# Kernel tuning notes

Hardware: AMD Instinct MI355X
Metric: run time of the kernel (lower is better)

## Reference

```python
import jax, jax.numpy as jnp
import numpy as np

NB_HEAD = 8
SIZE_PER_HEAD = 64
MAX_LEN = 1024
D_IN = 512
BATCH = 8
NEG_BIG = 1e12  # matches the torch module's mask * 1000000000000.0


def setup_inputs() -> dict:
    key = jax.random.key(0)
    ks = jax.random.split(key, 6)
    return {
        "Q_seq": jax.random.normal(ks[0], (BATCH, MAX_LEN, D_IN), dtype=jnp.float32),
        "K_seq": jax.random.normal(ks[1], (BATCH, MAX_LEN, D_IN), dtype=jnp.float32),
        "V_seq": jax.random.normal(ks[2], (BATCH, MAX_LEN, D_IN), dtype=jnp.float32),
        "WQ": jax.random.normal(ks[3], (D_IN, NB_HEAD * SIZE_PER_HEAD), dtype=jnp.float32),
        "WK": jax.random.normal(ks[4], (D_IN, NB_HEAD * SIZE_PER_HEAD), dtype=jnp.float32),
        "WV": jax.random.normal(ks[5], (D_IN, NB_HEAD * SIZE_PER_HEAD), dtype=jnp.float32),
    }


def reference(Q_seq, K_seq, V_seq, WQ, WK, WV):
    B, L, _ = Q_seq.shape
    H, D = NB_HEAD, SIZE_PER_HEAD
    # QKV projections -> [B, H, L, D]
    q = (Q_seq @ WQ).reshape(B, L, H, D).transpose(0, 2, 1, 3)
    k = (K_seq @ WK).reshape(B, L, H, D).transpose(0, 2, 1, 3)
    v = (V_seq @ WV).reshape(B, L, H, D).transpose(0, 2, 1, 3)
    # scaled dot-product scores [B, H, Lq, Lk]
    scores = jnp.einsum("bhqd,bhkd->bhqk", q, k) / jnp.sqrt(jnp.float32(D))
    # causal mask: the torch Mask() subtracts 1e12 where key_idx > query_idx
    causal = jnp.triu(jnp.ones((L, L), dtype=scores.dtype), k=1)  # 1 where k > q
    scores = scores - causal[None, None, :, :] * NEG_BIG
    attn = jax.nn.softmax(scores, axis=-1)
    out = jnp.einsum("bhqk,bhkd->bhqd", attn, v)  # [B, H, L, D]
    return out.transpose(0, 2, 1, 3).reshape(B, L, H * D)
```

## Files before the change

### kernel.cpp

```cpp
#include <hip/hip_runtime.h>
#include <cstddef>

#define LEN    1024
#define DIN    512
#define NHEAD  8
#define HDIM   64
#define BATCH  8

typedef __attribute__((ext_vector_type(8))) short  short8;
typedef __attribute__((ext_vector_type(4))) float  f32x4;

#define MFMA16(a, b, c) __builtin_amdgcn_mfma_f32_16x16x32_bf16((a), (b), (c), 0, 0, 0)
#define PERM_HI 0x07060302u
#define PERM_LO 0x05040100u

__device__ __forceinline__ unsigned short bf_hi(float x) {
    unsigned u = __float_as_uint(x);
    return (unsigned short)((u + 0x7fffu + ((u >> 16) & 1u)) >> 16);
}
__device__ __forceinline__ void bf_split(float x, unsigned short& h, unsigned short& l) {
    unsigned u  = __float_as_uint(x);
    unsigned hu = (u + 0x7fffu + ((u >> 16) & 1u)) >> 16;
    h = (unsigned short)hu;
    l = bf_hi(x - __uint_as_float(hu << 16));
}
__device__ __forceinline__ void unpack4(uint4 u, ushort4& h, ushort4& l) {
    h = make_ushort4((unsigned short)(u.x >> 16), (unsigned short)(u.y >> 16),
                     (unsigned short)(u.z >> 16), (unsigned short)(u.w >> 16));
    l = make_ushort4((unsigned short)(u.x & 0xffff), (unsigned short)(u.y & 0xffff),
                     (unsigned short)(u.z & 0xffff), (unsigned short)(u.w & 0xffff));
}
__device__ __forceinline__ void unpack8(uint4 a, uint4 b, uint4& h, uint4& l) {
    h = make_uint4(__builtin_amdgcn_perm(a.y, a.x, PERM_HI),
                   __builtin_amdgcn_perm(a.w, a.z, PERM_HI),
                   __builtin_amdgcn_perm(b.y, b.x, PERM_HI),
                   __builtin_amdgcn_perm(b.w, b.z, PERM_HI));
    l = make_uint4(__builtin_amdgcn_perm(a.y, a.x, PERM_LO),
                   __builtin_amdgcn_perm(a.w, a.z, PERM_LO),
                   __builtin_amdgcn_perm(b.y, b.x, PERM_LO),
                   __builtin_amdgcn_perm(b.w, b.z, PERM_LO));
}

template<int CTRL>
__device__ __forceinline__ float dpp_mov(float x) {
    return __int_as_float(__builtin_amdgcn_update_dpp(
        0, __float_as_int(x), CTRL, 0xF, 0xF, true));
}
__device__ __forceinline__ float red16_max(float x) {
    x = fmaxf(x, dpp_mov<0xB1>(x));
    x = fmaxf(x, dpp_mov<0x4E>(x));
    x = fmaxf(x, dpp_mov<0x141>(x));
    x = fmaxf(x, dpp_mov<0x140>(x));
    return x;
}
__device__ __forceinline__ float red16_sum(float x) {
    x += dpp_mov<0xB1>(x);
    x += dpp_mov<0x4E>(x);
    x += dpp_mov<0x141>(x);
    x += dpp_mov<0x140>(x);
    return x;
}

__global__ __launch_bounds__(256)
void wprep(const float* __restrict__ WQ, const float* __restrict__ WK,
           const float* __restrict__ WV, unsigned short* __restrict__ wt)
{
    __shared__ float T[64][68];
    const int z = blockIdx.z;
    const float* W = (z == 0) ? WQ : (z == 1) ? WK : WV;
    unsigned short* Wth = wt + (size_t)z * 524288;
    unsigned short* Wtl = Wth + 262144;
    const int k0 = blockIdx.x * 64, n0 = blockIdx.y * 64;
    const int t = threadIdx.x;
    #pragma unroll
    for (int e = 0; e < 4; ++e) {
        int f = e * 256 + t, r = f >> 4, c4 = (f & 15) << 2;
        *(float4*)&T[r][c4] = *(const float4*)&W[(size_t)(k0 + r) * 512 + n0 + c4];
    }
    __syncthreads();
    #pragma unroll
    for (int e = 0; e < 4; ++e) {
        int f = e * 256 + t, nr = f >> 4, kc4 = (f & 15) << 2;
        ushort4 h, l;
        bf_split(T[kc4 + 0][nr], h.x, l.x);
        bf_split(T[kc4 + 1][nr], h.y, l.y);
        bf_split(T[kc4 + 2][nr], h.z, l.z);
        bf_split(T[kc4 + 3][nr], h.w, l.w);
        *(ushort4*)&Wth[(size_t)(n0 + nr) * 512 + k0 + kc4] = h;
        *(ushort4*)&Wtl[(size_t)(n0 + nr) * 512 + k0 + kc4] = l;
    }
}

#define PSTR 40

__global__ __launch_bounds__(256, 3)
void proj_mfma(const float* __restrict__ Qin, const float* __restrict__ Kin,
               const float* __restrict__ Vin, const unsigned short* __restrict__ wt,
               unsigned int* __restrict__ qhl, unsigned int* __restrict__ khl,
               unsigned short* __restrict__ vh)
{
    __shared__ unsigned short Ah[128 * PSTR], Al[128 * PSTR],
                              Bh[128 * PSTR], Bl[128 * PSTR];
    const int z = blockIdx.z;
    const bool full = (z < 2);
    const float* X = (z == 0) ? Qin : (z == 1) ? Kin : Vin;
    const unsigned short* Wth = wt + (size_t)z * 524288;
    const unsigned short* Wtl = Wth + 262144;

    const int t = threadIdx.x, lane = t & 63, w = t >> 6;
    const int wm = w & 1, wn = w >> 1;
    const int m0 = blockIdx.x * 128, n0 = blockIdx.y * 128;
    const int lm = lane & 15, lq = lane >> 4;
    const int ar = t >> 1, ak = (t & 1) * 16;

    const float* Xp = X + (size_t)(m0 + ar) * 512 + ak;
    const unsigned short* Bph = Wth + (size_t)(n0 + ar) * 512 + ak;
    const unsigned short* Bpl = Wtl + (size_t)(n0 + ar) * 512 + ak;

    f32x4 acc[4][4];
    #pragma unroll
    for (int i = 0; i < 4; ++i)
        #pragma unroll
        for (int j = 0; j < 4; ++j) acc[i][j] = 0.f;

    float4 av[4];
    uint4 bh0, bh1, bl0, bl1;
    #pragma unroll
    for (int e = 0; e < 4; ++e) av[e] = *(const float4*)(Xp + e * 4);
    bh0 = *(const uint4*)(Bph);
    bh1 = *(const uint4*)(Bph + 8);
    if (full) { bl0 = *(const uint4*)(Bpl); bl1 = *(const uint4*)(Bpl + 8); }

    for (int k0 = 0; k0 < 512; k0 += 32) {
        __syncthreads();
        {
            const float* ff = (const float*)&av[0];
            uint hw[16];
            #pragma unroll
            for (int i = 0; i < 16; ++i) hw[i] = __float_as_uint(ff[i]) & 0xffff0000u;
            uint4 ahv  = make_uint4(__builtin_amdgcn_perm(hw[1],  hw[0],  PERM_HI),
                                    __builtin_amdgcn_perm(hw[3],  hw[2],  PERM_HI),
                                    __builtin_amdgcn_perm(hw[5],  hw[4],  PERM_HI),
                                    __builtin_amdgcn_perm(hw[7],  hw[6],  PERM_HI));
            uint4 ahv2 = make_uint4(__builtin_amdgcn_perm(hw[9],  hw[8],  PERM_HI),
                                    __builtin_amdgcn_perm(hw[11], hw[10], PERM_HI),
                                    __builtin_amdgcn_perm(hw[13], hw[12], PERM_HI),
                                    __builtin_amdgcn_perm(hw[15], hw[14], PERM_HI));
            *(uint4*)&Ah[ar * PSTR + ak]     = ahv;
            *(uint4*)&Ah[ar * PSTR + ak + 8] = ahv2;
            if (full) {
                uint lo[8];
                #pragma unroll
                for (int i = 0; i < 8; ++i) {
                    float r0 = ff[2*i]   - __uint_as_float(hw[2*i]);
                    float r1 = ff[2*i+1] - __uint_as_float(hw[2*i+1]);
                    lo[i] = ((uint)bf_hi(r1) << 16) | bf_hi(r0);
                }
                *(uint4*)&Al[ar * PSTR + ak]     = make_uint4(lo[0], lo[1], lo[2], lo[3]);
                *(uint4*)&Al[ar * PSTR + ak + 8] = make_uint4(lo[4], lo[5], lo[6], lo[7]);
            }
        }
        *(uint4*)&Bh[ar * PSTR + ak]     = bh0;
        *(uint4*)&Bh[ar * PSTR + ak + 8] = bh1;
        if (full) {
            *(uint4*)&Bl[ar * PSTR + ak]     = bl0;
            *(uint4*)&Bl[ar * PSTR + ak + 8] = bl1;
        }
        __syncthreads();

        if (k0 + 32 < 512) {
            #pragma unroll
            for (int e = 0; e < 4; ++e) av[e] = *(const float4*)(Xp + k0 + 32 + e * 4);
            bh0 = *(const uint4*)(Bph + k0 + 32);
            bh1 = *(const uint4*)(Bph + k0 + 40);
            if (full) {
                bl0 = *(const uint4*)(Bpl + k0 + 32);
                bl1 = *(const uint4*)(Bpl + k0 + 40);
            }
        }

        short8 a_h[4], a_l[4];
        #pragma unroll
        for (int mi = 0; mi < 4; ++mi) {
            int off = (wm * 64 + mi * 16 + lm) * PSTR + lq * 8;
            a_h[mi] = *(const short8*)&Ah[off];
            if (full) a_l[mi] = *(const short8*)&Al[off];
        }
        #pragma unroll
        for (int ni = 0; ni < 4; ++ni) {
            int off = (wn * 64 + ni * 16 + lm) * PSTR + lq * 8;
            short8 b_h = *(const short8*)&Bh[off];
            if (full) {
                short8 b_l = *(const short8*)&Bl[off];
                #pragma unroll
                for (int mi = 0; mi < 4; ++mi) {
                    acc[mi][ni] = MFMA16(a_l[mi], b_h, acc[mi][ni]);
                    acc[mi][ni] = MFMA16(a_h[mi], b_l, acc[mi][ni]);
                    acc[mi][ni] = MFMA16(a_h[mi], b_h, acc[mi][ni]);
                }
            } else {
                #pragma unroll
                for (int mi = 0; mi < 4; ++mi)
                    acc[mi][ni] = MFMA16(a_h[mi], b_h, acc[mi][ni]);
            }
        }
    }

    if (z < 2) {
        unsigned int* o = (z == 0) ? qhl : khl;
        const float sc = (z == 0) ? 0.18033688011112042f : 1.0f;
        #pragma unroll
        for (int mi = 0; mi < 4; ++mi)
            #pragma unroll
            for (int ni = 0; ni < 4; ++ni) {
                int n_abs = n0 + wn * 64 + ni * 16 + lm;
                int hd = n_abs >> 6, d = n_abs & 63;
                #pragma unroll
                for (int r = 0; r < 4; ++r) {
                    int m_abs = m0 + wm * 64 + mi * 16 + lq * 4 + r;
                    int b = m_abs >> 10, li = m_abs & 1023;
                    unsigned short hv, lv;
                    bf_split(acc[mi][ni][r] * sc, hv, lv);
                    o[(((size_t)b * NHEAD + hd) * LEN + li) * HDIM + d] =
                        ((unsigned)hv << 16) | lv;
                }
            }
    } else {
        #pragma unroll
        for (int mi = 0; mi < 4; ++mi) {
            int m_base = m0 + wm * 64 + mi * 16 + lq * 4;
            int b = m_base >> 10, l0 = m_base & 1023;
            #pragma unroll
            for (int ni = 0; ni < 4; ++ni) {
                int n_abs = n0 + wn * 64 + ni * 16 + lm;
                int hd = n_abs >> 6, d = n_abs & 63;
                ushort4 hv = make_ushort4(bf_hi(acc[mi][ni][0]), bf_hi(acc[mi][ni][1]),
                                          bf_hi(acc[mi][ni][2]), bf_hi(acc[mi][ni][3]));
                *(ushort4*)&vh[(((size_t)b * NHEAD + hd) * HDIM + d) * LEN + l0] = hv;
            }
        }
    }
}

__global__ __launch_bounds__(256)
void attn_mfma(const unsigned int* __restrict__ qhl, const unsigned int* __restrict__ khl,
               const unsigned short* __restrict__ vth, float* __restrict__ out)
{
    __shared__ unsigned short sm[18432];
    unsigned short* Kh  = sm;
    unsigned short* Kl  = sm + 4608;
    unsigned short* Pb  = sm;
    unsigned short* Vt  = sm + 9216;
    unsigned short* Qsh = sm;
    unsigned short* Qsl = sm + 9216;

    const int t = threadIdx.x, lane = t & 63, w = t >> 6;
    const int lm = lane & 15, lq = lane >> 4;
    const int bx = blockIdx.x;
    const int idx = bx >> 1, par = bx & 1;
    const int bh = idx & 63;
    const int a  = idx >> 6;
    const int qt = par ? (7 - a) : a;
    const size_t base = (size_t)bh * LEN * HDIM;
    const unsigned int*   qb = qhl + base;
    const unsigned int*   kb = khl + base;
    const unsigned short* vb = vth + base;
    const int Q0  = qt * 128;
    const int Q0w = Q0 + w * 32;

    #pragma unroll
    for (int e = 0; e < 8; ++e) {
        int f = e * 256 + t, r = f >> 4, c4 = (f & 15) << 2;
        uint4 u = *(const uint4*)&qb[(size_t)(Q0 + r) * 64 + c4];
        ushort4 h, l;
        unpack4(u, h, l);
        *(ushort4*)&Qsh[r * 72 + c4] = h;
        *(ushort4*)&Qsl[r * 72 + c4] = l;
    }
    __syncthreads();
    short8 qfh[2][2], qfl[2][2];
    #pragma unroll
    for (int mi = 0; mi < 2; ++mi)
        #pragma unroll
        for (int ks = 0; ks < 2; ++ks) {
            int off = (w * 32 + mi * 16 + lm) * 72 + ks * 32 + lq * 8;
            qfh[mi][ks] = *(const short8*)&Qsh[off];
            qfl[mi][ks] = *(const short8*)&Qsl[off];
        }

    float m_i[2][4], l_i[2][4];
    f32x4 oacc[2][4];
    #pragma unroll
    for (int mi = 0; mi < 2; ++mi)
        #pragma unroll
        for (int r = 0; r < 4; ++r) { m_i[mi][r] = -1e30f; l_i[mi][r] = 0.f; }
    #pragma unroll
    for (int mi = 0; mi < 2; ++mi)
        #pragma unroll
        for (int nd = 0; nd < 4; ++nd) oacc[mi][nd] = 0.f;

    const int kr = t >> 2, kq = t & 3;
    const int vd_ = t >> 3, vs8 = (t & 7) << 3;

    uint4 kreg[4], vreg[2];
    #pragma unroll
    for (int e = 0; e < 4; ++e)
        kreg[e] = *(const uint4*)&kb[(size_t)kr * 64 + kq * 16 + e * 4];
    #pragma unroll
    for (int e = 0; e < 2; ++e)
        vreg[e] = *(const uint4*)&vb[(size_t)(e * 32 + vd_) * LEN + vs8];

    const int jend = 2 * qt + 1;
    for (int jb = 0; jb <= jend; ++jb) {
        __syncthreads();
        {
            uint4 h0, l0, h1, l1;
            unpack8(kreg[0], kreg[1], h0, l0);
            unpack8(kreg[2], kreg[3], h1, l1);
            int ko = kr * 72 + kq * 16;
            *(uint4*)&Kh[ko]     = h0;
            *(uint4*)&Kh[ko + 8] = h1;
            *(uint4*)&Kl[ko]     = l0;
            *(uint4*)&Kl[ko + 8] = l1;
            *(uint4*)&Vt[(vd_)      * 72 + vs8] = vreg[0];
            *(uint4*)&Vt[(vd_ + 32) * 72 + vs8] = vreg[1];
        }
        __syncthreads();

        if (jb < jend) {
            #pragma unroll
            for (int e = 0; e < 4; ++e)
                kreg[e] = *(const uint4*)&kb[(size_t)((jb + 1) * 64 + kr) * 64 + kq * 16 + e * 4];
            #pragma unroll
            for (int e = 0; e < 2; ++e)
                vreg[e] = *(const uint4*)&vb[(size_t)(e * 32 + vd_) * LEN + (jb + 1) * 64 + vs8];
        }

        const bool active = (jb * 64 <= Q0w + 31);
        f32x4 sf[2][4];
        if (active) {
            #pragma unroll
            for (int mi = 0; mi < 2; ++mi)
                #pragma unroll
                for (int ni = 0; ni < 4; ++ni) sf[mi][ni] = 0.f;
            #pragma unroll
            for (int ks = 0; ks < 2; ++ks)
                #pragma unroll
                for (int ni = 0; ni < 4; ++ni) {
                    int off = (ni * 16 + lm) * 72 + ks * 32 + lq * 8;
                    short8 b_h = *(const short8*)&Kh[off];
                    short8 b_l = *(const short8*)&Kl[off];
                    #pragma unroll
                    for (int mi = 0; mi < 2; ++mi) {
                        sf[mi][ni] = MFMA16(qfl[mi][ks], b_h, sf[mi][ni]);
                        sf[mi][ni] = MFMA16(qfh[mi][ks], b_l, sf[mi][ni]);
                        sf[mi][ni] = MFMA16(qfh[mi][ks], b_h, sf[mi][ni]);
                    }
                }
            if (jb * 64 + 63 > Q0w) {
                #pragma unroll
                for (int mi = 0; mi < 2; ++mi)
                    #pragma unroll
                    for (int ni = 0; ni < 4; ++ni) {
                        int key = jb * 64 + ni * 16 + lm;
                        #pragma unroll
                        for (int r = 0; r < 4; ++r) {
                            int qi = Q0w + mi * 16 + lq * 4 + r;
                            if (key > qi) sf[mi][ni][r] = -1e30f;
                        }
                    }
            }
        }
        __syncthreads();

        if (active) {
            #pragma unroll
            for (int mi = 0; mi < 2; ++mi)
                #pragma unroll
                for (int r = 0; r < 4; ++r) {
                    float mv = fmaxf(fmaxf(sf[mi][0][r], sf[mi][1][r]),
                                     fmaxf(sf[mi][2][r], sf[mi][3][r]));
                    mv = red16_max(mv);
                    float mo = m_i[mi][r];
                    float mn = fmaxf(mo, mv);
                    float al = __builtin_amdgcn_exp2f(mo - mn);
                    m_i[mi][r] = mn;
                    float rs = 0.f;
                    int prow = (w * 32 + mi * 16 + lq * 4 + r) * 72 + lm;
                    #pragma unroll
                    for (int ni = 0; ni < 4; ++ni) {
                        float p = __builtin_amdgcn_exp2f(sf[mi][ni][r] - mn);
                        rs += p;
                        Pb[prow + ni * 16] = bf_hi(p);
                    }
                    rs = red16_sum(rs);
                    l_i[mi][r] = l_i[mi][r] * al + rs;
                    #pragma unroll
                    for (int nd = 0; nd < 4; ++nd) oacc[mi][nd][r] *= al;
                }
            short8 pf[2][2];
            #pragma unroll
            for (int mi = 0; mi < 2; ++mi)
                #pragma unroll
                for (int ks = 0; ks < 2; ++ks)
                    pf[mi][ks] = *(const short8*)&Pb[(w * 32 + mi * 16 + lm) * 72 + ks * 32 + lq * 8];
            #pragma unroll
            for (int ks = 0; ks < 2; ++ks)
                #pragma unroll
                for (int nd = 0; nd < 4; ++nd) {
                    short8 vf = *(const short8*)&Vt[(nd * 16 + lm) * 72 + ks * 32 + lq * 8];
                    #pragma unroll
                    for (int mi = 0; mi < 2; ++mi)
                        oacc[mi][nd] = MFMA16(pf[mi][ks], vf, oacc[mi][nd]);
                }
        }
    }

    const int b = bh >> 3, hd = bh & 7;
    #pragma unroll
    for (int mi = 0; mi < 2; ++mi)
        #pragma unroll
        for (int r = 0; r < 4; ++r) {
            int qrow = Q0w + mi * 16 + lq * 4 + r;
            float inv = 1.0f / l_i[mi][r];
            #pragma unroll
            for (int nd = 0; nd < 4; ++nd) {
                int d = nd * 16 + lm;
                out[((size_t)b * LEN + qrow) * (NHEAD * HDIM) + hd * 64 + d] =
                    oacc[mi][nd][r] * inv;
            }
        }
}

extern "C" void kernel_launch(void* const* d_in, const int* in_sizes, int n_in,
                              void* d_out, int out_size, void* d_ws, size_t ws_size,
                              hipStream_t stream)
{
    const float* Qin = (const float*)d_in[0];
    const float* Kin = (const float*)d_in[1];
    const float* Vin = (const float*)d_in[2];
    const float* WQ  = (const float*)d_in[3];
    const float* WK  = (const float*)d_in[4];
    const float* WV  = (const float*)d_in[5];

    const size_t per = (size_t)BATCH * NHEAD * LEN * HDIM;
    unsigned int*   qhl = (unsigned int*)d_ws;
    unsigned int*   khl = qhl + per;
    unsigned short* vh  = (unsigned short*)(khl + per);
    unsigned short* wt  = vh + per;

    wprep    <<<dim3(8, 8, 3),  256, 0, stream>>>(WQ, WK, WV, wt);
    proj_mfma<<<dim3(64, 4, 3), 256, 0, stream>>>(Qin, Kin, Vin, wt, qhl, khl, vh);
    attn_mfma<<<dim3(512),      256, 0, stream>>>(qhl, khl, vh, (float*)d_out);
}
```

Before: 185.4 us.

## Pre-split activations into bf16 hi/lo in a separate pass before projection GEMM

Adds an xprep kernel that converts the Q/K/V fp32 activations once into bf16 high and low halves in workspace. The projection GEMM then loads ready-made bf16 tiles instead of reading fp32 and splitting them inside every tile. Previously each activation row was re-read and re-split by all four N-blocks, so this removes repeated conversion work and halves the bytes loaded per tile. In exchange it adds an extra launch plus a write and re-read of the split activations. LDS stride drops from 40 to 36 and occupancy hint rises from 3 to 4 blocks.

Result: slower. 288.8 us (+55.8%).

```diff
diff --git a/kernel.cpp b/kernel.cpp
--- a/kernel.cpp
+++ b/kernel.cpp
@@ -91,11 +91,41 @@
     }
 }
 
-#define PSTR 40
-
-__global__ __launch_bounds__(256, 3)
-void proj_mfma(const float* __restrict__ Qin, const float* __restrict__ Kin,
-               const float* __restrict__ Vin, const unsigned short* __restrict__ wt,
+__global__ __launch_bounds__(256)
+void xprep(const float* __restrict__ Qin, const float* __restrict__ Kin,
+           const float* __restrict__ Vin,
+           unsigned short* __restrict__ xh, unsigned short* __restrict__ xl)
+{
+    const int z = blockIdx.y;
+    const float* X = (z == 0) ? Qin : (z == 1) ? Kin : Vin;
+    unsigned short* H = xh + (size_t)z * (8192 * 512);
+    unsigned short* L = xl + (size_t)z * (8192 * 512);
+    const size_t i = ((size_t)blockIdx.x * 256 + threadIdx.x) * 8;
+    float4 a = *(const float4*)&X[i];
+    float4 b = *(const float4*)&X[i + 4];
+    ushort4 h0, l0, h1, l1;
+    bf_split(a.x, h0.x, l0.x);
+    bf_split(a.y, h0.y, l0.y);
+    bf_split(a.z, h0.z, l0.z);
+    bf_split(a.w, h0.w, l0.w);
+    bf_split(b.x, h1.x, l1.x);
+    bf_split(b.y, h1.y, l1.y);
+    bf_split(b.z, h1.z, l1.z);
+    bf_split(b.w, h1.w, l1.w);
+    *(ushort4*)&H[i]     = h0;
+    *(ushort4*)&H[i + 4] = h1;
+    if (z < 2) {
+        *(ushort4*)&L[i]     = l0;
+        *(ushort4*)&L[i + 4] = l1;
+    }
+}
+
+#define PSTR 36
+
+__global__ __launch_bounds__(256, 4)
+void proj_mfma(const unsigned short* __restrict__ xh,
+               const unsigned short* __restrict__ xl,
+               const unsigned short* __restrict__ wt,
                unsigned int* __restrict__ qhl, unsigned int* __restrict__ khl,
                unsigned short* __restrict__ vh)
 {
@@ -103,7 +133,8 @@
                               Bh[128 * PSTR], Bl[128 * PSTR];
     const int z = blockIdx.z;
     const bool full = (z < 2);
-    const float* X = (z == 0) ? Qin : (z == 1) ? Kin : Vin;
+    const unsigned short* Xh  = xh + (size_t)z * (8192 * 512);
+    const unsigned short* Xl  = xl + (size_t)z * (8192 * 512);
     const unsigned short* Wth = wt + (size_t)z * 524288;
     const unsigned short* Wtl = Wth + 262144;
 
@@ -113,7 +144,8 @@
     const int lm = lane & 15, lq = lane >> 4;
     const int ar = t >> 1, ak = (t & 1) * 16;
 
-    const float* Xp = X + (size_t)(m0 + ar) * 512 + ak;
+    const unsigned short* Aph = Xh  + (size_t)(m0 + ar) * 512 + ak;
+    const unsigned short* Apl = Xl  + (size_t)(m0 + ar) * 512 + ak;
     const unsigned short* Bph = Wth + (size_t)(n0 + ar) * 512 + ak;
     const unsigned short* Bpl = Wtl + (size_t)(n0 + ar) * 512 + ak;
 
@@ -123,59 +155,42 @@
         #pragma unroll
         for (int j = 0; j < 4; ++j) acc[i][j] = 0.f;
 
-    float4 av[4];
-    uint4 bh0, bh1, bl0, bl1;
-    #pragma unroll
-    for (int e = 0; e < 4; ++e) av[e] = *(const float4*)(Xp + e * 4);
-    bh0 = *(const uint4*)(Bph);
-    bh1 = *(const uint4*)(Bph + 8);
-    if (full) { bl0 = *(const uint4*)(Bpl); bl1 = *(const uint4*)(Bpl + 8); }
+    uint4 pah0, pah1, pbh0, pbh1, pal0, pal1, pbl0, pbl1;
+    pah0 = *(const uint4*)(Aph);
+    pah1 = *(const uint4*)(Aph + 8);
+    pbh0 = *(const uint4*)(Bph);
+    pbh1 = *(const uint4*)(Bph + 8);
+    if (full) {
+        pal0 = *(const uint4*)(Apl);
+        pal1 = *(const uint4*)(Apl + 8);
+        pbl0 = *(const uint4*)(Bpl);
+        pbl1 = *(const uint4*)(Bpl + 8);
+    }
 
     for (int k0 = 0; k0 < 512; k0 += 32) {
         __syncthreads();
-        {
-            const float* ff = (const float*)&av[0];
-            uint hw[16];
-            #pragma unroll
-            for (int i = 0; i < 16; ++i) hw[i] = __float_as_uint(ff[i]) & 0xffff0000u;
-            uint4 ahv  = make_uint4(__builtin_amdgcn_perm(hw[1],  hw[0],  PERM_HI),
-                                    __builtin_amdgcn_perm(hw[3],  hw[2],  PERM_HI),
-                                    __builtin_amdgcn_perm(hw[5],  hw[4],  PERM_HI),
-                                    __builtin_amdgcn_perm(hw[7],  hw[6],  PERM_HI));
-            uint4 ahv2 = make_uint4(__builtin_amdgcn_perm(hw[9],  hw[8],  PERM_HI),
-                                    __builtin_amdgcn_perm(hw[11], hw[10], PERM_HI),
-                                    __builtin_amdgcn_perm(hw[13], hw[12], PERM_HI),
-                                    __builtin_amdgcn_perm(hw[15], hw[14], PERM_HI));
-            *(uint4*)&Ah[ar * PSTR + ak]     = ahv;
-            *(uint4*)&Ah[ar * PSTR + ak + 8] = ahv2;
+        *(uint4*)&Ah[ar * PSTR + ak]     = pah0;
+        *(uint4*)&Ah[ar * PSTR + ak + 8] = pah1;
+        *(uint4*)&Bh[ar * PSTR + ak]     = pbh0;
+        *(uint4*)&Bh[ar * PSTR + ak + 8] = pbh1;
+        if (full) {
+            *(uint4*)&Al[ar * PSTR + ak]     = pal0;
+            *(uint4*)&Al[ar * PSTR + ak + 8] = pal1;
+            *(uint4*)&Bl[ar * PSTR + ak]     = pbl0;
+            *(uint4*)&Bl[ar * PSTR + ak + 8] = pbl1;
+        }
+        __syncthreads();
+
+        if (k0 + 32 < 512) {
+            pah0 = *(const uint4*)(Aph + k0 + 32);
+            pah1 = *(const uint4*)(Aph + k0 + 40);
+            pbh0 = *(const uint4*)(Bph + k0 + 32);
+            pbh1 = *(const uint4*)(Bph + k0 + 40);
             if (full) {
-                uint lo[8];
-                #pragma unroll
-                for (int i = 0; i < 8; ++i) {
-                    float r0 = ff[2*i]   - __uint_as_float(hw[2*i]);
-                    float r1 = ff[2*i+1] - __uint_as_float(hw[2*i+1]);
-                    lo[i] = ((uint)bf_hi(r1) << 16) | bf_hi(r0);
-                }
-                *(uint4*)&Al[ar * PSTR + ak]     = make_uint4(lo[0], lo[1], lo[2], lo[3]);
-                *(uint4*)&Al[ar * PSTR + ak + 8] = make_uint4(lo[4], lo[5], lo[6], lo[7]);
-            }
-        }
-        *(uint4*)&Bh[ar * PSTR + ak]     = bh0;
-        *(uint4*)&Bh[ar * PSTR + ak + 8] = bh1;
-        if (full) {
-            *(uint4*)&Bl[ar * PSTR + ak]     = bl0;
-            *(uint4*)&Bl[ar * PSTR + ak + 8] = bl1;
-        }
-        __syncthreads();
-
-        if (k0 + 32 < 512) {
-            #pragma unroll
-            for (int e = 0; e < 4; ++e) av[e] = *(const float4*)(Xp + k0 + 32 + e * 4);
-            bh0 = *(const uint4*)(Bph + k0 + 32);
-            bh1 = *(const uint4*)(Bph + k0 + 40);
-            if (full) {
-                bl0 = *(const uint4*)(Bpl + k0 + 32);
-                bl1 = *(const uint4*)(Bpl + k0 + 40);
+                pal0 = *(const uint4*)(Apl + k0 + 32);
+                pal1 = *(const uint4*)(Apl + k0 + 40);
+                pbl0 = *(const uint4*)(Bpl + k0 + 32);
+                pbl1 = *(const uint4*)(Bpl + k0 + 40);
             }
         }
 
@@ -448,8 +463,11 @@
     unsigned int*   khl = qhl + per;
     unsigned short* vh  = (unsigned short*)(khl + per);
     unsigned short* wt  = vh + per;
-
-    wprep    <<<dim3(8, 8, 3),  256, 0, stream>>>(WQ, WK, WV, wt);
-    proj_mfma<<<dim3(64, 4, 3), 256, 0, stream>>>(Qin, Kin, Vin, wt, qhl, khl, vh);
-    attn_mfma<<<dim3(512),      256, 0, stream>>>(qhl, khl, vh, (float*)d_out);
-}
+    unsigned short* xh  = wt + (size_t)3 * 524288;
+    unsigned short* xl  = xh + (size_t)3 * per;
+
+    wprep    <<<dim3(8, 8, 3),   256, 0, stream>>>(WQ, WK, WV, wt);
+    xprep    <<<dim3(2048, 3),   256, 0, stream>>>(Qin, Kin, Vin, xh, xl);
+    proj_mfma<<<dim3(64, 4, 3),  256, 0, stream>>>(xh, xl, wt, qhl, khl, vh);
+    attn_mfma<<<dim3(512),       256, 0, stream>>>(qhl, khl, vh, (float*)d_out);
+}
```
